# Kernel optimization log

Hardware: AMD Instinct MI355X
Metric: run time of the kernel (lower is better)

## Reference

```python
import jax, jax.numpy as jnp
import numpy as np

N_ROW = 50000
N_COL = 50000
E = 1_200_000
D_IN = 64
D_H = 128


def _gconv(h_src, src, dst, w_e, W, b, n_src, n_dst):
    """DGL GraphConv(norm='both') with edge weights: symmetric degree norm
    (unweighted degrees, clamped to >=1), u_mul_e message, sum reduce, then linear."""
    ones = jnp.ones_like(w_e)
    out_deg = jnp.clip(jax.ops.segment_sum(ones, src, num_segments=n_src), 1.0)
    in_deg = jnp.clip(jax.ops.segment_sum(ones, dst, num_segments=n_dst), 1.0)
    hs = h_src * jax.lax.rsqrt(out_deg)[:, None]          # [n_src, F] pre-norm
    m = hs[src] * w_e[:, None]                            # [E, F] gather + edge weight
    agg = jax.ops.segment_sum(m, dst, num_segments=n_dst)  # [n_dst, F] scatter-sum
    agg = agg * jax.lax.rsqrt(in_deg)[:, None]
    return agg @ W + b


def setup_inputs() -> dict:
    key = jax.random.key(0)
    ks = jax.random.split(key, 16)
    return {
        'feat_row': jax.random.normal(ks[0], (N_ROW, D_IN), jnp.float32),
        'feat_col': jax.random.normal(ks[1], (N_COL, D_IN), jnp.float32),
        'src_rc': jax.random.randint(ks[2], (E,), 0, N_ROW),
        'dst_rc': jax.random.randint(ks[3], (E,), 0, N_COL),
        'w_rc': jax.random.uniform(ks[4], (E,), jnp.float32),
        'src_cr': jax.random.randint(ks[5], (E,), 0, N_COL),
        'dst_cr': jax.random.randint(ks[6], (E,), 0, N_ROW),
        'w_cr': jax.random.uniform(ks[7], (E,), jnp.float32),
        'W0_rc': jax.random.normal(ks[8], (D_IN, D_H), jnp.float32) / np.float32(np.sqrt(D_IN)),
        'b0_rc': jnp.zeros((D_H,), jnp.float32),
        'W0_cr': jax.random.normal(ks[9], (D_IN, D_H), jnp.float32) / np.float32(np.sqrt(D_IN)),
        'b0_cr': jnp.zeros((D_H,), jnp.float32),
        'W1_rc': jax.random.normal(ks[10], (D_H, D_H), jnp.float32) / np.float32(np.sqrt(D_H)),
        'b1_rc': jnp.zeros((D_H,), jnp.float32),
        'W1_cr': jax.random.normal(ks[11], (D_H, D_H), jnp.float32) / np.float32(np.sqrt(D_H)),
        'b1_cr': jnp.zeros((D_H,), jnp.float32),
    }


def reference(feat_row, feat_col, src_rc, dst_rc, w_rc, src_cr, dst_cr, w_cr,
              W0_rc, b0_rc, W0_cr, b0_cr, W1_rc, b1_rc, W1_cr, b1_cr):
    # Layer 1 (HeteroGraphConv, sum across relations; each dst type has one relation) + ReLU
    h_col1 = jax.nn.relu(_gconv(feat_row, src_rc, dst_rc, w_rc, W0_rc, b0_rc, N_ROW, N_COL))
    h_row1 = jax.nn.relu(_gconv(feat_col, src_cr, dst_cr, w_cr, W0_cr, b0_cr, N_COL, N_ROW))
    # Layer 2 + ReLU
    h_col2 = jax.nn.relu(_gconv(h_row1, src_rc, dst_rc, w_rc, W1_rc, b1_rc, N_ROW, N_COL))
    h_row2 = jax.nn.relu(_gconv(h_col1, src_cr, dst_cr, w_cr, W1_cr, b1_cr, N_COL, N_ROW))
    # dgl.mean_nodes per ntype (single graph -> [1, D_H]), summed over ntypes
    hg = jnp.mean(h_row2, axis=0, keepdims=True) + jnp.mean(h_col2, axis=0, keepdims=True)
    return hg
```

## Files before the change

kernel.cpp:

```cpp
#include <hip/hip_runtime.h>
#include <stdint.h>

constexpr int NROW = 50000;
constexpr int NCOL = 50000;
constexpr int DH   = 128;
constexpr int NTAB = 200000;
constexpr int HB   = 12500;
constexpr int HBLK = 64;
constexpr int DGRID = 1250;
constexpr int GGRID = 2048;
constexpr int CH    = 500;

typedef __attribute__((ext_vector_type(8))) short short8;
typedef __attribute__((ext_vector_type(4))) float f32x4;
typedef __attribute__((ext_vector_type(2))) float f32x2;

__device__ __forceinline__ float bf_hi(unsigned u) { return __uint_as_float(u & 0xffff0000u); }
__device__ __forceinline__ unsigned short f2bf(float f) {
    unsigned u = __float_as_uint(f);
    return (unsigned short)((u + 0x7fffu + ((u >> 16) & 1u)) >> 16);
}

__device__ __forceinline__ unsigned char f2fp8(float f) {
    unsigned b = __float_as_uint(f);
    unsigned s = (b >> 24) & 0x80u;
    unsigned mag = b & 0x7fffffffu;
    if (mag >= 0x43e00000u) return (unsigned char)(s | 0x7eu);
    unsigned r = mag + 0x7ffffu + ((mag >> 20) & 1u);
    int e = (int)(r >> 23) - 120;
    if (e < 1) {
        float af = __uint_as_float(mag);
        unsigned m = (unsigned)(af * 512.f + 0.5f);
        if (m > 8u) m = 8u;
        return (unsigned char)(s | m);
    }
    return (unsigned char)(s | (unsigned)(e << 3) | ((r >> 20) & 7u));
}

#if defined(__has_builtin) && __has_builtin(__builtin_amdgcn_cvt_pk_f32_fp8)
__device__ __forceinline__ f32x2 fp8x2f(unsigned v) {
    return __builtin_amdgcn_cvt_pk_f32_fp8((int)v, false);
}
#else
__device__ __forceinline__ float fp8_1(unsigned u) {
    unsigned s = (u & 0x80u) << 24, em = u & 0x7fu;
    if (em >= 8u) return __uint_as_float(s | ((em + 960u) << 20));
    float v = (float)em * 0.001953125f;
    return (u & 0x80u) ? -v : v;
}
__device__ __forceinline__ f32x2 fp8x2f(unsigned v) {
    f32x2 r; r.x = fp8_1(v & 0xffu); r.y = fp8_1((v >> 8) & 0xffu); return r;
}
#endif

__global__ __launch_bounds__(512) void hist_lds(
        const int* __restrict__ s_rc, const int* __restrict__ d_rc,
        const int* __restrict__ s_cr, const int* __restrict__ d_cr,
        unsigned short* __restrict__ partial, int E) {
    __shared__ int h[HB];
    const int sec = blockIdx.x >> 6;
    const int blk = blockIdx.x & (HBLK - 1);
    const int tab = sec >> 2;
    const int lo  = (sec & 3) * HB;
    const int* __restrict__ arr = (tab == 0) ? s_rc : (tab == 1) ? d_rc
                                 : (tab == 2) ? s_cr : d_cr;
    for (int i = threadIdx.x; i < HB; i += blockDim.x) h[i] = 0;
    __syncthreads();
    const int stride = HBLK * blockDim.x;
    for (int i = blk * blockDim.x + threadIdx.x; i < E; i += stride) {
        int id = arr[i] - lo;
        if ((unsigned)id < (unsigned)HB) atomicAdd(&h[id], 1);
    }
    __syncthreads();
    unsigned short* __restrict__ out = partial + ((size_t)sec * HBLK + blk) * HB;
    for (int i = threadIdx.x; i < HB; i += blockDim.x) out[i] = (unsigned short)h[i];
}

__global__ void reduce_norms2(const unsigned short* __restrict__ partial, int* __restrict__ cnt,
                              float* __restrict__ norms) {
    int stride = gridDim.x * blockDim.x;
    for (int i = blockIdx.x * blockDim.x + threadIdx.x; i < NTAB; i += stride) {
        int t = i / 50000;
        int r = i - t * 50000;
        int q = r / HB;
        int j = r - q * HB;
        const unsigned short* __restrict__ p = partial + ((size_t)(t * 4 + q) * HBLK) * HB + j;
        int s = 0;
#pragma unroll
        for (int b = 0; b < HBLK; ++b) s += p[(size_t)b * HB];
        cnt[i] = s;
        norms[i] = 1.0f / sqrtf((float)max(s, 1));
    }
}

__global__ __launch_bounds__(256) void scanA(const int* __restrict__ cnt, int* __restrict__ bsum) {
    __shared__ int red[256];
    const int c = blockIdx.x;
    const int* __restrict__ cbl = cnt + ((c >= 100) ? 150000 : 50000);
    const int j0 = (c % 100) * CH;
    int s = 0;
    for (int i = threadIdx.x; i < CH; i += 256) s += cbl[j0 + i];
    red[threadIdx.x] = s;
    __syncthreads();
    for (int off = 128; off > 0; off >>= 1) {
        if (threadIdx.x < off) red[threadIdx.x] += red[threadIdx.x + off];
        __syncthreads();
    }
    if (threadIdx.x == 0) bsum[c] = red[0];
}

__global__ void scanB(const int* __restrict__ bsum, int* __restrict__ cbase) {
    __shared__ int b[200];
    for (int i = threadIdx.x; i < 200; i += blockDim.x) b[i] = bsum[i];
    __syncthreads();
    if (threadIdx.x < 2) {
        int run = 0;
        const int o = threadIdx.x * 100;
        for (int k = 0; k < 100; ++k) { cbase[o + k] = run; run += b[o + k]; }
    }
}

__global__ __launch_bounds__(512) void scanC(const int* __restrict__ cnt,
                                             const int* __restrict__ cbase,
                                             int* __restrict__ ptr_rc, int* __restrict__ ptr_cr,
                                             int E) {
    __shared__ int buf[512];
    const int c = blockIdx.x;
    const int table = (c >= 100);
    const int* __restrict__ cbl = cnt + (table ? 150000 : 50000);
    int* __restrict__ ptr = table ? ptr_cr : ptr_rc;
    const int j0 = (c % 100) * CH;
    const int t = threadIdx.x;
    const int v = (t < CH) ? cbl[j0 + t] : 0;
    buf[t] = v;
    __syncthreads();
    for (int off = 1; off < 512; off <<= 1) {
        int tmp = (t >= off) ? buf[t - off] : 0;
        __syncthreads();
        buf[t] += tmp;
        __syncthreads();
    }
    if (t < CH) ptr[j0 + t] = cbase[c] + buf[t] - v;
    if ((c % 100) == 99 && t == 0) ptr[50000] = E;
}

__global__ void block_starts(const unsigned short* __restrict__ partial, int* __restrict__ bstart,
                             const int* __restrict__ ptr_rc, const int* __restrict__ ptr_cr) {
    int stride = gridDim.x * blockDim.x;
    for (int i = blockIdx.x * blockDim.x + threadIdx.x; i < 8 * HB; i += stride) {
        int fsec = i / HB;
        int j = i - fsec * HB;
        int rel = fsec >> 2, q = fsec & 3;
        int histsec = rel * 8 + 4 + q;
        const int* __restrict__ ptr = rel ? ptr_cr : ptr_rc;
        int run = ptr[q * HB + j];
        const unsigned short* __restrict__ p = partial + ((size_t)histsec * HBLK) * HB + j;
        int* __restrict__ o = bstart + ((size_t)fsec * HBLK) * HB + j;
#pragma unroll
        for (int b = 0; b < HBLK; ++b) {
            o[(size_t)b * HB] = run;
            run += p[(size_t)b * HB];
        }
    }
}

__global__ __launch_bounds__(512) void csr_fill_sorted(
        const int* __restrict__ sA, const int* __restrict__ dA,
        const float* __restrict__ wA, const float* __restrict__ routA, unsigned* __restrict__ pairA,
        const int* __restrict__ sB, const int* __restrict__ dB,
        const float* __restrict__ wB, const float* __restrict__ routB, unsigned* __restrict__ pairB,
        const int* __restrict__ bstart, int E) {
    __shared__ int offs[HB];
    const int fsec = blockIdx.x & 7;
    const int blk  = blockIdx.x >> 3;
    const int rel = fsec >> 2, q = fsec & 3;
    const int lo = q * HB;
    const int* __restrict__ src  = rel ? sB : sA;
    const int* __restrict__ dst  = rel ? dB : dA;
    const float* __restrict__ w  = rel ? wB : wA;
    const float* __restrict__ ro = rel ? routB : routA;
    unsigned* __restrict__ pair  = rel ? pairB : pairA;
    const int* __restrict__ bs = bstart + ((size_t)fsec * HBLK + blk) * HB;
    for (int i = threadIdx.x; i < HB; i += blockDim.x) offs[i] = bs[i];
    __syncthreads();
    const int stride = HBLK * blockDim.x;
    for (int i = blk * blockDim.x + threadIdx.x; i < E; i += stride) {
        int id = dst[i] - lo;
        if ((unsigned)id < (unsigned)HB) {
            int pos = atomicAdd(&offs[id], 1);
            int s = src[i];
            pair[pos] = (unsigned)s | ((unsigned)f2bf(w[i] * ro[s]) << 16);
        }
    }
}

__global__ void prep_tables(const float4* __restrict__ fr, const float4* __restrict__ fc,
                            unsigned* __restrict__ f8r, unsigned* __restrict__ f8c, int nq,
                            const float* __restrict__ W0a, const float* __restrict__ W0b,
                            const float* __restrict__ W1a, const float* __restrict__ W1b,
                            unsigned short* __restrict__ wt) {
    const int total = 2 * nq + 49152;
    int stride = gridDim.x * blockDim.x;
    for (int i = blockIdx.x * blockDim.x + threadIdx.x; i < total; i += stride) {
        if (i < 2 * nq) {
            bool second = i >= nq;
            int k = second ? i - nq : i;
            float4 v = second ? fc[k] : fr[k];
            unsigned o = (unsigned)f2fp8(v.x) | ((unsigned)f2fp8(v.y) << 8)
                       | ((unsigned)f2fp8(v.z) << 16) | ((unsigned)f2fp8(v.w) << 24);
            if (second) f8c[k] = o; else f8r[k] = o;
        } else {
            int j = i - 2 * nq;
            const float* W; int K, base;
            if (j < 8192)       { W = W0a; K = 64;  base = 0; }
            else if (j < 16384) { W = W0b; K = 64;  base = 8192;  j -= 8192; }
            else if (j < 32768) { W = W1a; K = 128; base = 16384; j -= 16384; }
            else                { W = W1b; K = 128; base = 32768; j -= 32768; }
            int n = j / K, k = j - n * K;
            wt[base + n * K + k] = f2bf(W[k * DH + n]);
        }
    }
}

__global__ void gather64_2(const uint8_t* __restrict__ hA, const int* __restrict__ ptrA,
                           const unsigned* __restrict__ pairA, unsigned short* __restrict__ aggA,
                           const uint8_t* __restrict__ hB, const int* __restrict__ ptrB,
                           const unsigned* __restrict__ pairB, unsigned short* __restrict__ aggB,
                           int n) {
    const int low  = blockIdx.x & 7;
    const int rel  = low >> 2;
    const int bid  = (blockIdx.x >> 3) * 4 + (low & 3);
    const uint8_t* __restrict__ h = rel ? hB : hA;
    const int* __restrict__ ptr  = rel ? ptrB : ptrA;
    const unsigned* __restrict__ pair = rel ? pairB : pairA;
    unsigned short* __restrict__ agg  = rel ? aggB : aggA;
    const int gw   = (bid * blockDim.x + threadIdx.x) >> 6;
    const int nw   = (GGRID * blockDim.x) >> 6;
    const int lane = threadIdx.x & 63;
    const int half = lane >> 5;
    const int c    = (lane & 31) << 1;
    for (int node = gw; node < n; node += nw) {
        const int beg = ptr[node], end = ptr[node + 1];
        float ax0 = 0.f, ay0 = 0.f, ax1 = 0.f, ay1 = 0.f;
        float ax2 = 0.f, ay2 = 0.f, ax3 = 0.f, ay3 = 0.f;
        int j = beg + half;
        for (; j + 6 < end; j += 8) {
            unsigned p0 = pair[j], p1 = pair[j + 2], p2 = pair[j + 4], p3 = pair[j + 6];
            unsigned h0 = *reinterpret_cast<const unsigned short*>(&h[(size_t)(p0 & 0xffffu) * 64 + c]);
            unsigned h1 = *reinterpret_cast<const unsigned short*>(&h[(size_t)(p1 & 0xffffu) * 64 + c]);
            unsigned h2 = *reinterpret_cast<const unsigned short*>(&h[(size_t)(p2 & 0xffffu) * 64 + c]);
            unsigned h3 = *reinterpret_cast<const unsigned short*>(&h[(size_t)(p3 & 0xffffu) * 64 + c]);
            f32x2 d0 = fp8x2f(h0), d1 = fp8x2f(h1), d2 = fp8x2f(h2), d3 = fp8x2f(h3);
            float w0 = bf_hi(p0), w1 = bf_hi(p1), w2 = bf_hi(p2), w3 = bf_hi(p3);
            ax0 = fmaf(d0.x, w0, ax0); ay0 = fmaf(d0.y, w0, ay0);
            ax1 = fmaf(d1.x, w1, ax1); ay1 = fmaf(d1.y, w1, ay1);
            ax2 = fmaf(d2.x, w2, ax2); ay2 = fmaf(d2.y, w2, ay2);
            ax3 = fmaf(d3.x, w3, ax3); ay3 = fmaf(d3.y, w3, ay3);
        }
        for (; j < end; j += 2) {
            unsigned p = pair[j];
            unsigned hv = *reinterpret_cast<const unsigned short*>(&h[(size_t)(p & 0xffffu) * 64 + c]);
            f32x2 d = fp8x2f(hv);
            float w = bf_hi(p);
            ax0 = fmaf(d.x, w, ax0); ay0 = fmaf(d.y, w, ay0);
        }
        float ax = (ax0 + ax1) + (ax2 + ax3);
        float ay = (ay0 + ay1) + (ay2 + ay3);
        ax += __shfl_xor(ax, 32);
        ay += __shfl_xor(ay, 32);
        if (half == 0) {
            unsigned pk = (unsigned)f2bf(ax) | ((unsigned)f2bf(ay) << 16);
            *reinterpret_cast<unsigned*>(&agg[(size_t)node * 64 + c]) = pk;
        }
    }
}

__global__ __launch_bounds__(256) void dense64_2(
        const unsigned short* __restrict__ aggA, const float* __restrict__ rinA,
        const unsigned short* __restrict__ wtA, const float* __restrict__ bA,
        unsigned short* __restrict__ outA,
        const unsigned short* __restrict__ aggB, const float* __restrict__ rinB,
        const unsigned short* __restrict__ wtB, const float* __restrict__ bB,
        unsigned short* __restrict__ outB, int n) {
    constexpr int K = 64, NCH = 2;
    const int rel = blockIdx.x >= DGRID;
    const int bid = rel ? blockIdx.x - DGRID : blockIdx.x;
    const unsigned short* __restrict__ agg = rel ? aggB : aggA;
    const float* __restrict__ rin = rel ? rinB : rinA;
    const unsigned short* __restrict__ wt = rel ? wtB : wtA;
    const float* __restrict__ b = rel ? bB : bA;
    unsigned short* __restrict__ outbf = rel ? outB : outA;

    const int wave = threadIdx.x >> 6;
    const int lane = threadIdx.x & 63;
    const int lrow = lane & 15;
    const int kgrp = lane >> 4;
    const int c0   = wave * 32;

    short8 bfr[2][NCH];
#pragma unroll
    for (int t = 0; t < 2; ++t)
#pragma unroll
        for (int ch = 0; ch < NCH; ++ch)
            bfr[t][ch] = *reinterpret_cast<const short8*>(
                &wt[(size_t)(c0 + t * 16 + lrow) * K + ch * 32 + kgrp * 8]);

    const float bias0 = b[c0 + lrow], bias1 = b[c0 + 16 + lrow];
    const int nstrip = n >> 4;
    for (int s = bid; s < nstrip; s += DGRID) {
        const int r0 = s << 4;
        f32x4 d0 = {0.f, 0.f, 0.f, 0.f}, d1 = {0.f, 0.f, 0.f, 0.f};
#pragma unroll
        for (int ch = 0; ch < NCH; ++ch) {
            short8 af = *reinterpret_cast<const short8*>(
                &agg[(size_t)(r0 + lrow) * K + ch * 32 + kgrp * 8]);
            d0 = __builtin_amdgcn_mfma_f32_16x16x32_bf16(af, bfr[0][ch], d0, 0, 0, 0);
            d1 = __builtin_amdgcn_mfma_f32_16x16x32_bf16(af, bfr[1][ch], d1, 0, 0, 0);
        }
#pragma unroll
        for (int i = 0; i < 4; ++i) {
            const int row = r0 + kgrp * 4 + i;
            const float rv = rin[row];
            outbf[(size_t)row * DH + c0 + lrow]      = f2bf(fmaxf(fmaf(rv, d0[i], bias0), 0.f));
            outbf[(size_t)row * DH + c0 + 16 + lrow] = f2bf(fmaxf(fmaf(rv, d1[i], bias1), 0.f));
        }
    }
}

__global__ __launch_bounds__(256) void h1t_gemm2(
        const unsigned short* __restrict__ hA, const unsigned short* __restrict__ wtA,
        uint8_t* __restrict__ htA,
        const unsigned short* __restrict__ hB, const unsigned short* __restrict__ wtB,
        uint8_t* __restrict__ htB, int n) {
    constexpr int K = 128, NCH = 4;
    const int rel = blockIdx.x >= DGRID;
    const int bid = rel ? blockIdx.x - DGRID : blockIdx.x;
    const unsigned short* __restrict__ h = rel ? hB : hA;
    const unsigned short* __restrict__ wt = rel ? wtB : wtA;
    uint8_t* __restrict__ ht = rel ? htB : htA;

    const int wave = threadIdx.x >> 6;
    const int lane = threadIdx.x & 63;
    const int lrow = lane & 15;
    const int kgrp = lane >> 4;
    const int c0   = wave * 32;

    short8 bfr[2][NCH];
#pragma unroll
    for (int t = 0; t < 2; ++t)
#pragma unroll
        for (int ch = 0; ch < NCH; ++ch)
            bfr[t][ch] = *reinterpret_cast<const short8*>(
                &wt[(size_t)(c0 + t * 16 + lrow) * K + ch * 32 + kgrp * 8]);

    const int nstrip = n >> 4;
    for (int s = bid; s < nstrip; s += DGRID) {
        const int r0 = s << 4;
        f32x4 d0 = {0.f, 0.f, 0.f, 0.f}, d1 = {0.f, 0.f, 0.f, 0.f};
#pragma unroll
        for (int ch = 0; ch < NCH; ++ch) {
            short8 af = *reinterpret_cast<const short8*>(
                &h[(size_t)(r0 + lrow) * K + ch * 32 + kgrp * 8]);
            d0 = __builtin_amdgcn_mfma_f32_16x16x32_bf16(af, bfr[0][ch], d0, 0, 0, 0);
            d1 = __builtin_amdgcn_mfma_f32_16x16x32_bf16(af, bfr[1][ch], d1, 0, 0, 0);
        }
#pragma unroll
        for (int i = 0; i < 4; ++i) {
            const int row = r0 + kgrp * 4 + i;
            ht[(size_t)row * DH + c0 + lrow]      = f2fp8(d0[i]);
            ht[(size_t)row * DH + c0 + 16 + lrow] = f2fp8(d1[i]);
        }
    }
}

__global__ __launch_bounds__(256) void gather_final(
        const uint8_t* __restrict__ htA, const int* __restrict__ ptrA,
        const unsigned* __restrict__ pairA, const float* __restrict__ rinA,
        const float* __restrict__ bA,
        const uint8_t* __restrict__ htB, const int* __restrict__ ptrB,
        const unsigned* __restrict__ pairB, const float* __restrict__ rinB,
        const float* __restrict__ bB,
        float* __restrict__ partsum, int n, float invn) {
    const int low  = blockIdx.x & 7;
    const int rel  = low >> 2;
    const int bid  = (blockIdx.x >> 3) * 4 + (low & 3);
    const uint8_t* __restrict__ ht = rel ? htB : htA;
    const int* __restrict__ ptr  = rel ? ptrB : ptrA;
    const unsigned* __restrict__ pair = rel ? pairB : pairA;
    const float* __restrict__ rin = rel ? rinB : rinA;
    const float* __restrict__ b   = rel ? bB : bA;

    const int gw   = (bid * blockDim.x + threadIdx.x) >> 6;
    const int nw   = (GGRID * blockDim.x) >> 6;
    const int lane = threadIdx.x & 63;
    const int c    = lane << 1;
    const float bias0 = b[c], bias1 = b[c + 1];
    float m0 = 0.f, m1 = 0.f;

    for (int node = gw; node < n; node += nw) {
        const int beg = ptr[node], end = ptr[node + 1];
        float ax[8], ay[8];
#pragma unroll
        for (int u = 0; u < 8; ++u) { ax[u] = 0.f; ay[u] = 0.f; }
        int j = beg;
        for (; j + 7 < end; j += 8) {
            unsigned p[8]; unsigned hv[8];
#pragma unroll
            for (int u = 0; u < 8; ++u) p[u] = pair[j + u];
#pragma unroll
            for (int u = 0; u < 8; ++u)
                hv[u] = *reinterpret_cast<const unsigned short*>(&ht[(size_t)(p[u] & 0xffffu) * 128 + c]);
#pragma unroll
            for (int u = 0; u < 8; ++u) {
                f32x2 d = fp8x2f(hv[u]);
                float w = bf_hi(p[u]);
                ax[u] = fmaf(d.x, w, ax[u]);
                ay[u] = fmaf(d.y, w, ay[u]);
            }
        }
        for (; j < end; ++j) {
            unsigned p = pair[j];
            unsigned hv = *reinterpret_cast<const unsigned short*>(&ht[(size_t)(p & 0xffffu) * 128 + c]);
            f32x2 d = fp8x2f(hv);
            float w = bf_hi(p);
            ax[0] = fmaf(d.x, w, ax[0]); ay[0] = fmaf(d.y, w, ay[0]);
        }
        float accx = ((ax[0] + ax[1]) + (ax[2] + ax[3])) + ((ax[4] + ax[5]) + (ax[6] + ax[7]));
        float accy = ((ay[0] + ay[1]) + (ay[2] + ay[3])) + ((ay[4] + ay[5]) + (ay[6] + ay[7]));
        const float rv = rin[node];
        m0 += fmaxf(fmaf(rv, accx, bias0), 0.f);
        m1 += fmaxf(fmaf(rv, accy, bias1), 0.f);
    }

    __shared__ float red[512];
    red[threadIdx.x] = m0;
    red[256 + threadIdx.x] = m1;
    __syncthreads();
    if (threadIdx.x < 64) {
        float s0 = red[threadIdx.x] + red[threadIdx.x + 64] + red[threadIdx.x + 128] + red[threadIdx.x + 192];
        float s1 = red[256 + threadIdx.x] + red[256 + threadIdx.x + 64]
                 + red[256 + threadIdx.x + 128] + red[256 + threadIdx.x + 192];
        float* part = partsum + (size_t)blockIdx.x * DH;
        part[2 * threadIdx.x]     = s0 * invn;
        part[2 * threadIdx.x + 1] = s1 * invn;
    }
}

__global__ void reduce_out(const float* __restrict__ partial, float* __restrict__ out, int nrows) {
    const int t = threadIdx.x;
    const int per = nrows / gridDim.x;
    const int b0 = blockIdx.x * per;
    float s = 0.f;
    for (int b = b0; b < b0 + per; ++b) s += partial[(size_t)b * DH + t];
    atomicAdd(&out[t], s);
}

extern "C" void kernel_launch(void* const* d_in, const int* in_sizes, int n_in,
                              void* d_out, int out_size, void* d_ws, size_t ws_size,
                              hipStream_t stream) {
    const float* feat_row = (const float*)d_in[0];
    const float* feat_col = (const float*)d_in[1];
    const int*   src_rc   = (const int*)d_in[2];
    const int*   dst_rc   = (const int*)d_in[3];
    const float* w_rc     = (const float*)d_in[4];
    const int*   src_cr   = (const int*)d_in[5];
    const int*   dst_cr   = (const int*)d_in[6];
    const float* w_cr     = (const float*)d_in[7];
    const float* W0_rc    = (const float*)d_in[8];
    const float* b0_rc    = (const float*)d_in[9];
    const float* W0_cr    = (const float*)d_in[10];
    const float* b0_cr    = (const float*)d_in[11];
    const float* W1_rc    = (const float*)d_in[12];
    const float* b1_rc    = (const float*)d_in[13];
    const float* W1_cr    = (const float*)d_in[14];
    const float* b1_cr    = (const float*)d_in[15];
    const int E = in_sizes[2];
    float* out = (float*)d_out;

    int*   cnt     = (int*)d_ws;
    float* norms   = (float*)(cnt + 200000);
    int*   ptr_rc  = (int*)(norms + 200000);
    int*   ptr_cr  = ptr_rc + 50004;
    int*   bsum    = ptr_cr + 50004;
    int*   cbase   = bsum + 200;
    unsigned* pair_rc = (unsigned*)(cbase + 216);
    unsigned* pair_cr = pair_rc + E;
    unsigned short* agg_col = (unsigned short*)(pair_cr + E);
    unsigned short* agg_row = agg_col + (size_t)NCOL * 64;
    uint8_t* f8_row = (uint8_t*)(agg_row + (size_t)NROW * 64);
    uint8_t* f8_col = f8_row + (size_t)NROW * 64;
    unsigned short* h_col1 = (unsigned short*)(f8_col + (size_t)NCOL * 64);
    unsigned short* h_row1 = h_col1 + (size_t)NCOL * DH;
    uint8_t* ht_row = (uint8_t*)(h_row1 + (size_t)NROW * DH);
    uint8_t* ht_col = ht_row + (size_t)NROW * DH;
    float* partsum = (float*)(ht_col + (size_t)NCOL * DH);
    unsigned short* wt = (unsigned short*)(partsum + (size_t)2 * GGRID * DH);
    unsigned short* partial = (unsigned short*)agg_col;
    int* bstart = (int*)(partial + (size_t)16 * HBLK * HB);

    float* r_out_rc = norms;
    float* r_in_rc  = norms + NROW;
    float* r_out_cr = norms + NROW + NCOL;
    float* r_in_cr  = norms + NROW + 2 * NCOL;

    unsigned short* wt0_rc = wt;
    unsigned short* wt0_cr = wt + 8192;
    unsigned short* wt1_rc = wt + 16384;
    unsigned short* wt1_cr = wt + 32768;

    hist_lds<<<16 * HBLK, 512, 0, stream>>>(src_rc, dst_rc, src_cr, dst_cr, partial, E);
    reduce_norms2<<<512, 256, 0, stream>>>(partial, cnt, norms);
    scanA<<<200, 256, 0, stream>>>(cnt, bsum);
    scanB<<<1, 256, 0, stream>>>(bsum, cbase);
    scanC<<<200, 512, 0, stream>>>(cnt, cbase, ptr_rc, ptr_cr, E);
    block_starts<<<400, 256, 0, stream>>>(partial, bstart, ptr_rc, ptr_cr);
    csr_fill_sorted<<<8 * HBLK, 512, 0, stream>>>(
        src_rc, dst_rc, w_rc, r_out_rc, pair_rc,
        src_cr, dst_cr, w_cr, r_out_cr, pair_cr, bstart, E);

    prep_tables<<<2048, 256, 0, stream>>>((const float4*)feat_row, (const float4*)feat_col,
                                          (unsigned*)f8_row, (unsigned*)f8_col, NROW * 64 / 4,
                                          W0_rc, W0_cr, W1_rc, W1_cr, wt);

    gather64_2<<<2 * GGRID, 256, 0, stream>>>(f8_row, ptr_rc, pair_rc, agg_col,
                                              f8_col, ptr_cr, pair_cr, agg_row, NCOL);
    dense64_2<<<2 * DGRID, 256, 0, stream>>>(agg_col, r_in_rc, wt0_rc, b0_rc, h_col1,
                                             agg_row, r_in_cr, wt0_cr, b0_cr, h_row1, NCOL);

    h1t_gemm2<<<2 * DGRID, 256, 0, stream>>>(h_row1, wt1_rc, ht_row,
                                             h_col1, wt1_cr, ht_col, NROW);
    hipMemsetAsync(out, 0, DH * sizeof(float), stream);
    gather_final<<<2 * GGRID, 256, 0, stream>>>(
        ht_row, ptr_rc, pair_rc, r_in_rc, b1_rc,
        ht_col, ptr_cr, pair_cr, r_in_cr, b1_cr,
        partsum, NCOL, 1.0f / NCOL);
    reduce_out<<<32, 128, 0, stream>>>(partsum, out, 2 * GGRID);
}
```

Baseline: 332.9 us.

## Repartition gather lanes: 4-byte fp8 loads in layer-1, channel-split halves in final gather

```diff
diff --git a/kernel.cpp b/kernel.cpp
--- a/kernel.cpp
+++ b/kernel.cpp
@@ -41,6 +41,11 @@
 __device__ __forceinline__ f32x2 fp8x2f(unsigned v) {
     return __builtin_amdgcn_cvt_pk_f32_fp8((int)v, false);
 }
+__device__ __forceinline__ f32x4 fp8x4f(unsigned v) {
+    f32x2 lo = __builtin_amdgcn_cvt_pk_f32_fp8((int)v, false);
+    f32x2 hi = __builtin_amdgcn_cvt_pk_f32_fp8((int)v, true);
+    f32x4 r; r.x = lo.x; r.y = lo.y; r.z = hi.x; r.w = hi.y; return r;
+}
 #else
 __device__ __forceinline__ float fp8_1(unsigned u) {
     unsigned s = (u & 0x80u) << 24, em = u & 0x7fu;
@@ -50,6 +55,10 @@
 }
 __device__ __forceinline__ f32x2 fp8x2f(unsigned v) {
     f32x2 r; r.x = fp8_1(v & 0xffu); r.y = fp8_1((v >> 8) & 0xffu); return r;
+}
+__device__ __forceinline__ f32x4 fp8x4f(unsigned v) {
+    f32x4 r; r.x = fp8_1(v & 0xffu); r.y = fp8_1((v >> 8) & 0xffu);
+    r.z = fp8_1((v >> 16) & 0xffu); r.w = fp8_1((v >> 24) & 0xffu); return r;
 }
 #endif
 
@@ -237,40 +246,42 @@
     const int gw   = (bid * blockDim.x + threadIdx.x) >> 6;
     const int nw   = (GGRID * blockDim.x) >> 6;
     const int lane = threadIdx.x & 63;
-    const int half = lane >> 5;
-    const int c    = (lane & 31) << 1;
+    const int qtr  = lane >> 4;
+    const unsigned coff = (unsigned)((lane & 15) << 2);
     for (int node = gw; node < n; node += nw) {
         const int beg = ptr[node], end = ptr[node + 1];
-        float ax0 = 0.f, ay0 = 0.f, ax1 = 0.f, ay1 = 0.f;
-        float ax2 = 0.f, ay2 = 0.f, ax3 = 0.f, ay3 = 0.f;
-        int j = beg + half;
-        for (; j + 6 < end; j += 8) {
-            unsigned p0 = pair[j], p1 = pair[j + 2], p2 = pair[j + 4], p3 = pair[j + 6];
-            unsigned h0 = *reinterpret_cast<const unsigned short*>(&h[(size_t)(p0 & 0xffffu) * 64 + c]);
-            unsigned h1 = *reinterpret_cast<const unsigned short*>(&h[(size_t)(p1 & 0xffffu) * 64 + c]);
-            unsigned h2 = *reinterpret_cast<const unsigned short*>(&h[(size_t)(p2 & 0xffffu) * 64 + c]);
-            unsigned h3 = *reinterpret_cast<const unsigned short*>(&h[(size_t)(p3 & 0xffffu) * 64 + c]);
-            f32x2 d0 = fp8x2f(h0), d1 = fp8x2f(h1), d2 = fp8x2f(h2), d3 = fp8x2f(h3);
-            float w0 = bf_hi(p0), w1 = bf_hi(p1), w2 = bf_hi(p2), w3 = bf_hi(p3);
-            ax0 = fmaf(d0.x, w0, ax0); ay0 = fmaf(d0.y, w0, ay0);
-            ax1 = fmaf(d1.x, w1, ax1); ay1 = fmaf(d1.y, w1, ay1);
-            ax2 = fmaf(d2.x, w2, ax2); ay2 = fmaf(d2.y, w2, ay2);
-            ax3 = fmaf(d3.x, w3, ax3); ay3 = fmaf(d3.y, w3, ay3);
-        }
-        for (; j < end; j += 2) {
+        float a0[2] = {0.f, 0.f}, a1[2] = {0.f, 0.f}, a2[2] = {0.f, 0.f}, a3[2] = {0.f, 0.f};
+        int j = beg + qtr;
+        for (; j + 4 < end; j += 8) {
+            unsigned p0 = pair[j], p1 = pair[j + 4];
+            unsigned hv0 = *reinterpret_cast<const unsigned*>(&h[((p0 & 0xffffu) << 6) + coff]);
+            unsigned hv1 = *reinterpret_cast<const unsigned*>(&h[((p1 & 0xffffu) << 6) + coff]);
+            f32x4 d0 = fp8x4f(hv0), d1 = fp8x4f(hv1);
+            float w0 = bf_hi(p0), w1 = bf_hi(p1);
+            a0[0] = fmaf(d0.x, w0, a0[0]); a1[0] = fmaf(d0.y, w0, a1[0]);
+            a2[0] = fmaf(d0.z, w0, a2[0]); a3[0] = fmaf(d0.w, w0, a3[0]);
+            a0[1] = fmaf(d1.x, w1, a0[1]); a1[1] = fmaf(d1.y, w1, a1[1]);
+            a2[1] = fmaf(d1.z, w1, a2[1]); a3[1] = fmaf(d1.w, w1, a3[1]);
+        }
+        for (; j < end; j += 4) {
             unsigned p = pair[j];
-            unsigned hv = *reinterpret_cast<const unsigned short*>(&h[(size_t)(p & 0xffffu) * 64 + c]);
-            f32x2 d = fp8x2f(hv);
+            unsigned hv = *reinterpret_cast<const unsigned*>(&h[((p & 0xffffu) << 6) + coff]);
+            f32x4 d = fp8x4f(hv);
             float w = bf_hi(p);
-            ax0 = fmaf(d.x, w, ax0); ay0 = fmaf(d.y, w, ay0);
-        }
-        float ax = (ax0 + ax1) + (ax2 + ax3);
-        float ay = (ay0 + ay1) + (ay2 + ay3);
-        ax += __shfl_xor(ax, 32);
-        ay += __shfl_xor(ay, 32);
-        if (half == 0) {
-            unsigned pk = (unsigned)f2bf(ax) | ((unsigned)f2bf(ay) << 16);
-            *reinterpret_cast<unsigned*>(&agg[(size_t)node * 64 + c]) = pk;
+            a0[0] = fmaf(d.x, w, a0[0]); a1[0] = fmaf(d.y, w, a1[0]);
+            a2[0] = fmaf(d.z, w, a2[0]); a3[0] = fmaf(d.w, w, a3[0]);
+        }
+        float s0 = a0[0] + a0[1], s1 = a1[0] + a1[1];
+        float s2 = a2[0] + a2[1], s3 = a3[0] + a3[1];
+        s0 += __shfl_xor(s0, 16); s0 += __shfl_xor(s0, 32);
+        s1 += __shfl_xor(s1, 16); s1 += __shfl_xor(s1, 32);
+        s2 += __shfl_xor(s2, 16); s2 += __shfl_xor(s2, 32);
+        s3 += __shfl_xor(s3, 16); s3 += __shfl_xor(s3, 32);
+        if (lane < 16) {
+            uint2 pk;
+            pk.x = (unsigned)f2bf(s0) | ((unsigned)f2bf(s1) << 16);
+            pk.y = (unsigned)f2bf(s2) | ((unsigned)f2bf(s3) << 16);
+            *reinterpret_cast<uint2*>(&agg[(size_t)node * 64 + ((lane & 15) << 2)]) = pk;
         }
     }
 }
@@ -383,7 +394,8 @@
         float* __restrict__ partsum, int n, float invn) {
     const int low  = blockIdx.x & 7;
     const int rel  = low >> 2;
-    const int bid  = (blockIdx.x >> 3) * 4 + (low & 3);
+    const int chf  = (low >> 1) & 1;
+    const int bid  = (blockIdx.x >> 3) * 2 + (low & 1);
     const uint8_t* __restrict__ ht = rel ? htB : htA;
     const int* __restrict__ ptr  = rel ? ptrB : ptrA;
     const unsigned* __restrict__ pair = rel ? pairB : pairA;
@@ -391,67 +403,69 @@
     const float* __restrict__ b   = rel ? bB : bA;
 
     const int gw   = (bid * blockDim.x + threadIdx.x) >> 6;
-    const int nw   = (GGRID * blockDim.x) >> 6;
+    const int nw   = ((GGRID / 2) * blockDim.x) >> 6;
     const int lane = threadIdx.x & 63;
-    const int c    = lane << 1;
-    const float bias0 = b[c], bias1 = b[c + 1];
+    const int h2   = lane >> 5;
+    const unsigned coff = (unsigned)(chf * 64 + ((lane & 31) << 1));
+    const float b0v = b[coff], b1v = b[coff + 1];
     float m0 = 0.f, m1 = 0.f;
 
     for (int node = gw; node < n; node += nw) {
         const int beg = ptr[node], end = ptr[node + 1];
-        float ax[8], ay[8];
-#pragma unroll
-        for (int u = 0; u < 8; ++u) { ax[u] = 0.f; ay[u] = 0.f; }
-        int j = beg;
-        for (; j + 7 < end; j += 8) {
-            unsigned p[8]; unsigned hv[8];
-#pragma unroll
-            for (int u = 0; u < 8; ++u) p[u] = pair[j + u];
-#pragma unroll
-            for (int u = 0; u < 8; ++u)
-                hv[u] = *reinterpret_cast<const unsigned short*>(&ht[(size_t)(p[u] & 0xffffu) * 128 + c]);
-#pragma unroll
-            for (int u = 0; u < 8; ++u) {
+        float a0[4] = {0.f, 0.f, 0.f, 0.f}, a1[4] = {0.f, 0.f, 0.f, 0.f};
+        int j = beg + h2;
+        for (; j + 6 < end; j += 8) {
+            unsigned p[4], hv[4];
+#pragma unroll
+            for (int u = 0; u < 4; ++u) p[u] = pair[j + 2 * u];
+#pragma unroll
+            for (int u = 0; u < 4; ++u)
+                hv[u] = *reinterpret_cast<const unsigned short*>(&ht[((p[u] & 0xffffu) << 7) + coff]);
+#pragma unroll
+            for (int u = 0; u < 4; ++u) {
                 f32x2 d = fp8x2f(hv[u]);
                 float w = bf_hi(p[u]);
-                ax[u] = fmaf(d.x, w, ax[u]);
-                ay[u] = fmaf(d.y, w, ay[u]);
+                a0[u] = fmaf(d.x, w, a0[u]);
+                a1[u] = fmaf(d.y, w, a1[u]);
             }
         }
-        for (; j < end; ++j) {
+        for (; j < end; j += 2) {
             unsigned p = pair[j];
-            unsigned hv = *reinterpret_cast<const unsigned short*>(&ht[(size_t)(p & 0xffffu) * 128 + c]);
+            unsigned hv = *reinterpret_cast<const unsigned short*>(&ht[((p & 0xffffu) << 7) + coff]);
             f32x2 d = fp8x2f(hv);
             float w = bf_hi(p);
-            ax[0] = fmaf(d.x, w, ax[0]); ay[0] = fmaf(d.y, w, ay[0]);
-        }
-        float accx = ((ax[0] + ax[1]) + (ax[2] + ax[3])) + ((ax[4] + ax[5]) + (ax[6] + ax[7]));
-        float accy = ((ay[0] + ay[1]) + (ay[2] + ay[3])) + ((ay[4] + ay[5]) + (ay[6] + ay[7]));
+            a0[0] = fmaf(d.x, w, a0[0]);
+            a1[0] = fmaf(d.y, w, a1[0]);
+        }
+        float sx = (a0[0] + a0[1]) + (a0[2] + a0[3]);
+        float sy = (a1[0] + a1[1]) + (a1[2] + a1[3]);
+        sx += __shfl_xor(sx, 32);
+        sy += __shfl_xor(sy, 32);
         const float rv = rin[node];
-        m0 += fmaxf(fmaf(rv, accx, bias0), 0.f);
-        m1 += fmaxf(fmaf(rv, accy, bias1), 0.f);
-    }
-
-    __shared__ float red[512];
-    red[threadIdx.x] = m0;
-    red[256 + threadIdx.x] = m1;
+        m0 += fmaxf(fmaf(rv, sx, b0v), 0.f);
+        m1 += fmaxf(fmaf(rv, sy, b1v), 0.f);
+    }
+
+    __shared__ float red[4][64];
+    const int wv = threadIdx.x >> 6;
+    if (h2 == 0) {
+        red[wv][(lane & 31) * 2]     = m0;
+        red[wv][(lane & 31) * 2 + 1] = m1;
+    }
     __syncthreads();
     if (threadIdx.x < 64) {
-        float s0 = red[threadIdx.x] + red[threadIdx.x + 64] + red[threadIdx.x + 128] + red[threadIdx.x + 192];
-        float s1 = red[256 + threadIdx.x] + red[256 + threadIdx.x + 64]
-                 + red[256 + threadIdx.x + 128] + red[256 + threadIdx.x + 192];
-        float* part = partsum + (size_t)blockIdx.x * DH;
-        part[2 * threadIdx.x]     = s0 * invn;
-        part[2 * threadIdx.x + 1] = s1 * invn;
-    }
-}
-
-__global__ void reduce_out(const float* __restrict__ partial, float* __restrict__ out, int nrows) {
+        float s = red[0][threadIdx.x] + red[1][threadIdx.x]
+                + red[2][threadIdx.x] + red[3][threadIdx.x];
+        partsum[(size_t)blockIdx.x * 64 + threadIdx.x] = s * invn;
+    }
+}
+
+__global__ void reduce_out2(const float* __restrict__ partsum, float* __restrict__ out, int nblk) {
     const int t = threadIdx.x;
-    const int per = nrows / gridDim.x;
-    const int b0 = blockIdx.x * per;
+    const int ch = t >> 6, c = t & 63;
     float s = 0.f;
-    for (int b = b0; b < b0 + per; ++b) s += partial[(size_t)b * DH + t];
+    for (int b = blockIdx.x; b < nblk; b += gridDim.x)
+        if (((b >> 1) & 1) == ch) s += partsum[(size_t)b * 64 + c];
     atomicAdd(&out[t], s);
 }
 
@@ -534,5 +548,5 @@
         ht_row, ptr_rc, pair_rc, r_in_rc, b1_rc,
         ht_col, ptr_cr, pair_cr, r_in_cr, b1_cr,
         partsum, NCOL, 1.0f / NCOL);
-    reduce_out<<<32, 128, 0, stream>>>(partsum, out, 2 * GGRID);
-}
+    reduce_out2<<<64, 128, 0, stream>>>(partsum, out, 2 * GGRID);
+}
```

Measured after the change: 347.0 us. 4.2% more time.
